# Optimization experiments

Hardware: AMD Instinct MI355X
Metric: run time of the kernel (lower is better)

## Reference

```python
import jax, jax.numpy as jnp
import numpy as np

N = 1024
B = 128
DT = 0.1
STEPS = 10

def setup_inputs() -> dict:
    key = jax.random.key(0)
    k1, k2, k3 = jax.random.split(key, 3)
    theta_init = jax.random.normal(k1, (B, N), dtype=jnp.float32)
    K0 = jax.random.normal(k2, (N, N), dtype=jnp.float32) * 0.1
    K = (K0 + K0.T) / 2  # symmetric coupling matrix, as in __init__
    omega = jax.random.normal(k3, (N,), dtype=jnp.float32) * 0.1
    K_global = jnp.asarray(0.5, dtype=jnp.float32)
    return {"theta_init": theta_init, "K": K, "omega": omega, "K_global": K_global}

def _compute_coherence(theta):
    # Kuramoto order parameter r = |<e^{i theta}>| over oscillator axis
    cos_mean = jnp.cos(theta).mean(axis=-1)
    sin_mean = jnp.sin(theta).mean(axis=-1)
    return jnp.sqrt(cos_mean ** 2 + sin_mean ** 2)

def reference(theta_init, K, omega, K_global):
    n = theta_init.shape[-1]

    def step(theta, _):
        # theta_diff[b, i, j] = theta[b, j] - theta[b, i]
        theta_diff = theta[..., None, :] - theta[..., :, None]  # [B, n, n]
        coupling_sum = (K * jnp.sin(theta_diff)).sum(axis=-1)   # [B, n]
        dtheta = omega + (K_global / n) * coupling_sum
        theta_new = theta + DT * dtheta
        # wrap to (-pi, pi]
        theta_new = jnp.arctan2(jnp.sin(theta_new), jnp.cos(theta_new))
        return theta_new, None

    theta, _ = jax.lax.scan(step, theta_init, None, length=STEPS)
    coherence = _compute_coherence(theta)
    return theta, coherence
```

## Files before the change

kernel.cpp:

```cpp
#include <hip/hip_runtime.h>
#include <math.h>

#define KN 1024
#define KB 128
#define KDT 0.1f
#define KSTEPS 10
#define KMAGIC 0x5A170000u
#define KPOISON 0xAAAAAAAAu
#define PI_F 3.14159265358979f
#define TWO_PI_F 6.28318530717959f

typedef __attribute__((ext_vector_type(8))) short short8;
typedef __attribute__((ext_vector_type(4))) float floatx4;
typedef unsigned long long u64;

__device__ __forceinline__ unsigned short f2bf(float f) {
    unsigned u = __float_as_uint(f);
    u += 0x7FFF + ((u >> 16) & 1);
    return (unsigned short)(u >> 16);
}

__device__ __forceinline__ unsigned xidx(int grp, int b15, int k) {
    return (unsigned)(grp * 16384 + (k >> 5) * 512 + ((k >> 1) & 3) * 128 +
                      ((k >> 3) & 3) * 32 + b15 * 2 + (k & 1));
}

__global__ __launch_bounds__(512)
void k_main(const float* __restrict__ theta0,
            const float* __restrict__ Kmat,
            const float* __restrict__ omega,
            const float* __restrict__ kg,
            float* __restrict__ out_theta,
            float* __restrict__ out_coh,
            unsigned* __restrict__ slots,
            float* __restrict__ acc,
            unsigned* __restrict__ xA,
            unsigned* __restrict__ xB)
{
    const int grp = blockIdx.x >> 5;
    const int b0  = grp * 16;
    const int i0  = (blockIdx.x & 31) * 32;

    const int tid  = threadIdx.x;
    const int lane = tid & 63;
    const int kq   = tid >> 6;
    const int r16  = lane & 15;
    const int quad = lane >> 4;

    __shared__ float ldsY[8][2][16][34];

    unsigned* cnt = &slots[grp * 32];
    unsigned* go  = &slots[256 + grp * 32];

    if ((blockIdx.x & 31) == 0 && tid < 16) {
        __hip_atomic_store(&acc[(b0 + tid) * 16], 0.f, __ATOMIC_RELAXED,
                           __HIP_MEMORY_SCOPE_AGENT);
        __hip_atomic_store(&acc[2048 + (b0 + tid) * 16], 0.f, __ATOMIC_RELAXED,
                           __HIP_MEMORY_SCOPE_AGENT);
    }

    short8 bfrag[2][4];
    #pragma unroll
    for (int wi = 0; wi < 2; ++wi) {
        const float* kp = Kmat + (size_t)(i0 + wi * 16 + r16) * KN + kq * 128 + quad * 8;
        #pragma unroll
        for (int it = 0; it < 4; ++it) {
            const float4 v0 = *reinterpret_cast<const float4*>(kp + it * 32);
            const float4 v1 = *reinterpret_cast<const float4*>(kp + it * 32 + 4);
            short8 b_;
            b_[0] = (short)f2bf(v0.x); b_[1] = (short)f2bf(v0.y);
            b_[2] = (short)f2bf(v0.z); b_[3] = (short)f2bf(v0.w);
            b_[4] = (short)f2bf(v1.x); b_[5] = (short)f2bf(v1.y);
            b_[6] = (short)f2bf(v1.z); b_[7] = (short)f2bf(v1.w);
            bfrag[wi][it] = b_;
        }
    }

    const int eb = b0 + (tid >> 5);
    const int ei = i0 + (tid & 31);
    float th_reg = theta0[(size_t)eb * KN + ei];
    const float omg = omega[ei];
    float sn, cs;
    __sincosf(th_reg, &sn, &cs);
    __hip_atomic_store(&xA[xidx(grp, eb & 15, ei)],
                       (unsigned)f2bf(sn) | ((unsigned)f2bf(cs) << 16),
                       __ATOMIC_RELAXED, __HIP_MEMORY_SCOPE_AGENT);
    const float scale = kg[0] * (1.0f / (float)KN);

    unsigned nbar = 0;
    auto arrive_wait = [&]() {
        ++nbar;
        __syncthreads();
        if (tid == 0) {
            unsigned old = __hip_atomic_fetch_add(cnt, 1u, __ATOMIC_RELAXED,
                                                  __HIP_MEMORY_SCOPE_AGENT);
            if (old == KPOISON + 32u * nbar - 1u) {
                __hip_atomic_store(go, KMAGIC + nbar, __ATOMIC_RELAXED,
                                   __HIP_MEMORY_SCOPE_AGENT);
            } else {
                unsigned polls = 0;
                while (__hip_atomic_load(go, __ATOMIC_RELAXED,
                                         __HIP_MEMORY_SCOPE_AGENT) != KMAGIC + nbar) {
                    __builtin_amdgcn_s_sleep(2);
                    if (++polls > 4000000u) break;
                }
            }
        }
        __syncthreads();
    };

    arrive_wait();

    const unsigned* xcur = xA;
    unsigned* xnxt = xB;
    float s2 = sn, c2 = cs;
    for (int s = 0; s < KSTEPS; ++s) {
        const u64* xg = (const u64*)xcur + grp * 8192 + kq * 1024 + lane;
        u64 aw[4][4];
        #pragma unroll
        for (int it = 0; it < 4; ++it)
            #pragma unroll
            for (int jj = 0; jj < 4; ++jj)
                aw[it][jj] = __hip_atomic_load((u64*)(xg + it * 256 + jj * 64),
                                               __ATOMIC_RELAXED,
                                               __HIP_MEMORY_SCOPE_AGENT);
        floatx4 accS[2] = {{0.f,0.f,0.f,0.f},{0.f,0.f,0.f,0.f}};
        floatx4 accC[2] = {{0.f,0.f,0.f,0.f},{0.f,0.f,0.f,0.f}};
        #pragma unroll
        for (int it = 0; it < 4; ++it) {
            short8 a_s, a_c;
            #pragma unroll
            for (int jj = 0; jj < 4; ++jj) {
                unsigned lo = (unsigned)aw[it][jj];
                unsigned hi = (unsigned)(aw[it][jj] >> 32);
                a_s[jj * 2]     = (short)(lo & 0xffffu);
                a_c[jj * 2]     = (short)(lo >> 16);
                a_s[jj * 2 + 1] = (short)(hi & 0xffffu);
                a_c[jj * 2 + 1] = (short)(hi >> 16);
            }
            #pragma unroll
            for (int wi = 0; wi < 2; ++wi) {
                accS[wi] = __builtin_amdgcn_mfma_f32_16x16x32_bf16(a_s, bfrag[wi][it], accS[wi], 0, 0, 0);
                accC[wi] = __builtin_amdgcn_mfma_f32_16x16x32_bf16(a_c, bfrag[wi][it], accC[wi], 0, 0, 0);
            }
        }
        #pragma unroll
        for (int wi = 0; wi < 2; ++wi)
            #pragma unroll
            for (int r = 0; r < 4; ++r) {
                ldsY[kq][0][quad * 4 + r][wi * 16 + r16] = accS[wi][r];
                ldsY[kq][1][quad * 4 + r][wi * 16 + r16] = accC[wi][r];
            }
        __syncthreads();

        {
            const int bl = tid >> 5, ilo = tid & 31;
            float Ys = 0.f, Yc = 0.f;
            #pragma unroll
            for (int q = 0; q < 8; ++q) {
                Ys += ldsY[q][0][bl][ilo];
                Yc += ldsY[q][1][bl][ilo];
            }
            const float coupling = cs * Ys - sn * Yc;
            float tn = th_reg + KDT * (omg + scale * coupling);
            __sincosf(tn, &s2, &c2);
            if (tn > PI_F)       tn -= TWO_PI_F;
            else if (tn < -PI_F) tn += TWO_PI_F;
            th_reg = tn;
            sn = s2; cs = c2;
        }
        if (s < KSTEPS - 1) {
            __hip_atomic_store(&xnxt[xidx(grp, eb & 15, ei)],
                               (unsigned)f2bf(s2) | ((unsigned)f2bf(c2) << 16),
                               __ATOMIC_RELAXED, __HIP_MEMORY_SCOPE_AGENT);
            arrive_wait();
            const unsigned* t = xcur; xcur = xnxt; xnxt = (unsigned*)t;
        } else {
            out_theta[(size_t)eb * KN + ei] = th_reg;
        }
    }

    __syncthreads();
    float* red = &ldsY[0][0][0][0];
    red[tid]       = s2;
    red[512 + tid] = c2;
    __syncthreads();
    if (tid < 16) {
        float ss = 0.f, cc = 0.f;
        #pragma unroll
        for (int il2 = 0; il2 < 32; ++il2) {
            ss += red[tid * 32 + il2];
            cc += red[512 + tid * 32 + il2];
        }
        atomicAdd(&acc[(b0 + tid) * 16], ss);
        atomicAdd(&acc[2048 + (b0 + tid) * 16], cc);
    }
    arrive_wait();
    if ((blockIdx.x & 31) == 0 && tid < 16) {
        float sv = __hip_atomic_load(&acc[(b0 + tid) * 16],
                                     __ATOMIC_RELAXED, __HIP_MEMORY_SCOPE_AGENT);
        float cv = __hip_atomic_load(&acc[2048 + (b0 + tid) * 16],
                                     __ATOMIC_RELAXED, __HIP_MEMORY_SCOPE_AGENT);
        float sm = sv * (1.0f / (float)KN);
        float cm = cv * (1.0f / (float)KN);
        out_coh[b0 + tid] = sqrtf(cm * cm + sm * sm);
    }
}

extern "C" void kernel_launch(void* const* d_in, const int* in_sizes, int n_in,
                              void* d_out, int out_size, void* d_ws, size_t ws_size,
                              hipStream_t stream)
{
    (void)in_sizes; (void)n_in; (void)out_size; (void)ws_size;

    const float* theta0 = (const float*)d_in[0];
    const float* Kmat   = (const float*)d_in[1];
    const float* omega  = (const float*)d_in[2];
    const float* kg     = (const float*)d_in[3];

    float* out_theta = (float*)d_out;
    float* out_coh   = out_theta + (size_t)KB * KN;

    unsigned* slots = (unsigned*)d_ws;
    float* acc      = (float*)((char*)d_ws + 4096);
    unsigned* xA    = (unsigned*)((char*)d_ws + 4096 + 16384);
    unsigned* xB    = xA + (size_t)KB * KN;

    k_main<<<256, 512, 0, stream>>>(theta0, Kmat, omega, kg,
                                    out_theta, out_coh, slots, acc, xA, xB);
}
```

Before: 99.72 us.

## Replace group counter barrier with per-block epoch flags polled per wave

```diff
diff --git a/kernel.cpp b/kernel.cpp
--- a/kernel.cpp
+++ b/kernel.cpp
@@ -5,8 +5,7 @@
 #define KB 128
 #define KDT 0.1f
 #define KSTEPS 10
-#define KMAGIC 0x5A170000u
-#define KPOISON 0xAAAAAAAAu
+#define KMAGIC 0xB0000000u
 #define PI_F 3.14159265358979f
 #define TWO_PI_F 6.28318530717959f
 
@@ -32,7 +31,7 @@
             const float* __restrict__ kg,
             float* __restrict__ out_theta,
             float* __restrict__ out_coh,
-            unsigned* __restrict__ slots,
+            unsigned* __restrict__ flags,
             float* __restrict__ acc,
             unsigned* __restrict__ xA,
             unsigned* __restrict__ xB)
@@ -48,9 +47,6 @@
     const int quad = lane >> 4;
 
     __shared__ float ldsY[8][2][16][34];
-
-    unsigned* cnt = &slots[grp * 32];
-    unsigned* go  = &slots[256 + grp * 32];
 
     if ((blockIdx.x & 31) == 0 && tid < 16) {
         __hip_atomic_store(&acc[(b0 + tid) * 16], 0.f, __ATOMIC_RELAXED,
@@ -87,34 +83,30 @@
                        __ATOMIC_RELAXED, __HIP_MEMORY_SCOPE_AGENT);
     const float scale = kg[0] * (1.0f / (float)KN);
 
-    unsigned nbar = 0;
-    auto arrive_wait = [&]() {
-        ++nbar;
-        __syncthreads();
-        if (tid == 0) {
-            unsigned old = __hip_atomic_fetch_add(cnt, 1u, __ATOMIC_RELAXED,
-                                                  __HIP_MEMORY_SCOPE_AGENT);
-            if (old == KPOISON + 32u * nbar - 1u) {
-                __hip_atomic_store(go, KMAGIC + nbar, __ATOMIC_RELAXED,
-                                   __HIP_MEMORY_SCOPE_AGENT);
-            } else {
-                unsigned polls = 0;
-                while (__hip_atomic_load(go, __ATOMIC_RELAXED,
-                                         __HIP_MEMORY_SCOPE_AGENT) != KMAGIC + nbar) {
-                    __builtin_amdgcn_s_sleep(2);
-                    if (++polls > 4000000u) break;
-                }
-            }
-        }
-        __syncthreads();
+    __syncthreads();
+    if (tid == 0)
+        __hip_atomic_store(&flags[blockIdx.x], KMAGIC + 0u,
+                           __ATOMIC_RELAXED, __HIP_MEMORY_SCOPE_AGENT);
+
+    auto wait_chunks = [&](unsigned tgt) {
+        unsigned polls = 0;
+        for (;;) {
+            unsigned v = tgt;
+            if (lane < 4)
+                v = __hip_atomic_load(&flags[grp * 32 + kq * 4 + lane],
+                                      __ATOMIC_RELAXED, __HIP_MEMORY_SCOPE_AGENT);
+            if (__ballot(v >= tgt) == ~0ull) break;
+            if (++polls > 4000000u) break;
+            __builtin_amdgcn_s_sleep(2);
+        }
     };
-
-    arrive_wait();
 
     const unsigned* xcur = xA;
     unsigned* xnxt = xB;
     float s2 = sn, c2 = cs;
     for (int s = 0; s < KSTEPS; ++s) {
+        wait_chunks(KMAGIC + (unsigned)s);
+
         const u64* xg = (const u64*)xcur + grp * 8192 + kq * 1024 + lane;
         u64 aw[4][4];
         #pragma unroll
@@ -173,7 +165,10 @@
             __hip_atomic_store(&xnxt[xidx(grp, eb & 15, ei)],
                                (unsigned)f2bf(s2) | ((unsigned)f2bf(c2) << 16),
                                __ATOMIC_RELAXED, __HIP_MEMORY_SCOPE_AGENT);
-            arrive_wait();
+            __syncthreads();
+            if (tid == 0)
+                __hip_atomic_store(&flags[blockIdx.x], KMAGIC + (unsigned)(s + 1),
+                                   __ATOMIC_RELAXED, __HIP_MEMORY_SCOPE_AGENT);
             const unsigned* t = xcur; xcur = xnxt; xnxt = (unsigned*)t;
         } else {
             out_theta[(size_t)eb * KN + ei] = th_reg;
@@ -195,15 +190,35 @@
         atomicAdd(&acc[(b0 + tid) * 16], ss);
         atomicAdd(&acc[2048 + (b0 + tid) * 16], cc);
     }
-    arrive_wait();
-    if ((blockIdx.x & 31) == 0 && tid < 16) {
-        float sv = __hip_atomic_load(&acc[(b0 + tid) * 16],
-                                     __ATOMIC_RELAXED, __HIP_MEMORY_SCOPE_AGENT);
-        float cv = __hip_atomic_load(&acc[2048 + (b0 + tid) * 16],
-                                     __ATOMIC_RELAXED, __HIP_MEMORY_SCOPE_AGENT);
-        float sm = sv * (1.0f / (float)KN);
-        float cm = cv * (1.0f / (float)KN);
-        out_coh[b0 + tid] = sqrtf(cm * cm + sm * sm);
+    __syncthreads();
+    if (tid == 0)
+        __hip_atomic_store(&flags[blockIdx.x], KMAGIC + (unsigned)KSTEPS,
+                           __ATOMIC_RELAXED, __HIP_MEMORY_SCOPE_AGENT);
+
+    if ((blockIdx.x & 31) == 0) {
+        if (tid < 64) {
+            const unsigned tgt = KMAGIC + (unsigned)KSTEPS;
+            unsigned polls = 0;
+            for (;;) {
+                unsigned v = tgt;
+                if (lane < 32)
+                    v = __hip_atomic_load(&flags[grp * 32 + lane],
+                                          __ATOMIC_RELAXED, __HIP_MEMORY_SCOPE_AGENT);
+                if (__ballot(v >= tgt) == ~0ull) break;
+                if (++polls > 4000000u) break;
+                __builtin_amdgcn_s_sleep(2);
+            }
+        }
+        __syncthreads();
+        if (tid < 16) {
+            float sv = __hip_atomic_load(&acc[(b0 + tid) * 16],
+                                         __ATOMIC_RELAXED, __HIP_MEMORY_SCOPE_AGENT);
+            float cv = __hip_atomic_load(&acc[2048 + (b0 + tid) * 16],
+                                         __ATOMIC_RELAXED, __HIP_MEMORY_SCOPE_AGENT);
+            float sm = sv * (1.0f / (float)KN);
+            float cm = cv * (1.0f / (float)KN);
+            out_coh[b0 + tid] = sqrtf(cm * cm + sm * sm);
+        }
     }
 }
 
@@ -221,11 +236,11 @@
     float* out_theta = (float*)d_out;
     float* out_coh   = out_theta + (size_t)KB * KN;
 
-    unsigned* slots = (unsigned*)d_ws;
+    unsigned* flags = (unsigned*)d_ws;
     float* acc      = (float*)((char*)d_ws + 4096);
     unsigned* xA    = (unsigned*)((char*)d_ws + 4096 + 16384);
     unsigned* xB    = xA + (size_t)KB * KN;
 
     k_main<<<256, 512, 0, stream>>>(theta0, Kmat, omega, kg,
-                                    out_theta, out_coh, slots, acc, xA, xB);
-}
+                                    out_theta, out_coh, flags, acc, xA, xB);
+}
```

After: 97.89 us. About the same (-1.8%).
